# Kernel optimization log

Measured on AMD Instinct MI355X. Metric: run time of the kernel, lower is better.

## Reference

```python
import jax, jax.numpy as jnp
import numpy as np

N_NODES = 50000
N_EDGES = 800000
IN_F, H_F, OUT_F = 256, 256, 128


def setup_inputs() -> dict:
    key = jax.random.key(0)
    k1, k2, k3, k4, k5, k6 = jax.random.split(key, 6)
    in_feat = jax.random.normal(k1, (N_NODES, IN_F), dtype=jnp.float32)
    src = jax.random.randint(k2, (N_EDGES,), 0, N_NODES, dtype=jnp.int32)
    dst = jax.random.randint(k3, (N_EDGES,), 0, N_NODES, dtype=jnp.int32)
    s1 = 1.0 / np.sqrt(IN_F)
    s2 = 1.0 / np.sqrt(H_F)
    W1 = jax.random.uniform(k4, (IN_F, H_F), dtype=jnp.float32, minval=-s1, maxval=s1)
    b1 = jnp.zeros((H_F,), dtype=jnp.float32)
    W2 = jax.random.uniform(k5, (H_F, OUT_F), dtype=jnp.float32, minval=-s2, maxval=s2)
    b2 = jnp.zeros((OUT_F,), dtype=jnp.float32)
    return {"in_feat": in_feat, "src": src, "dst": dst,
            "W1": W1, "b1": b1, "W2": W2, "b2": b2}


def _graph_conv(x, W, b, src, dst, n_nodes):
    # DGL GraphConv with norm='both':
    #   h = D_in^{-1/2} A D_out^{-1/2} (X W) + b   (degrees clamped to min 1)
    ones = jnp.ones((src.shape[0],), dtype=x.dtype)
    deg_out = jax.ops.segment_sum(ones, src, num_segments=n_nodes)
    deg_in = jax.ops.segment_sum(ones, dst, num_segments=n_nodes)
    norm_out = jax.lax.rsqrt(jnp.maximum(deg_out, 1.0))  # [N]
    norm_in = jax.lax.rsqrt(jnp.maximum(deg_in, 1.0))    # [N]
    h = (x @ W) * norm_out[:, None]                       # [N, F_out]
    agg = jax.ops.segment_sum(h[src], dst, num_segments=n_nodes)  # SpMM
    return agg * norm_in[:, None] + b


def reference(in_feat, src, dst, W1, b1, W2, b2):
    n = in_feat.shape[0]
    h = _graph_conv(in_feat, W1, b1, src, dst, n)
    h = jax.nn.relu(h)
    h = _graph_conv(h, W2, b2, src, dst, n)
    # dgl.mean_nodes over a single graph -> mean across all nodes
    return jnp.mean(h, axis=0)  # [OUT_F]
```

## Files before the change

kernel.cpp:

```cpp
#include <hip/hip_runtime.h>


#define NNODES 50000
#define NEDGES 800000
#define G1_BM   ((NNODES + 127) / 128)
#define MEGA_NB 3911
#define WS_NB   4096

typedef __bf16 bf16x8 __attribute__((ext_vector_type(8)));
typedef float f32x4 __attribute__((ext_vector_type(4)));
typedef float f32x2 __attribute__((ext_vector_type(2)));

__device__ __forceinline__ unsigned short f2b(float f) {
    union { float f; unsigned u; } v; v.f = f;
    unsigned r = 0x7fffu + ((v.u >> 16) & 1u);
    return (unsigned short)((v.u + r) >> 16);
}
__device__ __forceinline__ unsigned char f2fp8(float x) {
    return (unsigned char)(__builtin_amdgcn_cvt_pk_fp8_f32(x, x, 0, false) & 0xff);
}
__device__ __forceinline__ float rdeg(int d) {
    return __frsqrt_rn((float)max(d, 1));
}

__global__ void k_cast_w1(const float* __restrict__ W1, unsigned short* __restrict__ W1t,
                          int* __restrict__ deg0) {
    int id = blockIdx.x * blockDim.x + threadIdx.x;
    int k = id >> 8, n = id & 255;
    W1t[n * 256 + k] = f2b(W1[id]);
    deg0[id] = 0;
    int j = id + 65536;
    if (j < 2 * NNODES) deg0[j] = 0;
}

__global__ __launch_bounds__(256) void k_mega1(
    const int* __restrict__ src, const int* __restrict__ dst,
    int* __restrict__ degOut, int* __restrict__ degIn,
    unsigned short* __restrict__ col2, unsigned short* __restrict__ dst2,
    const float* __restrict__ X, const unsigned short* __restrict__ W1t,
    unsigned char* __restrict__ H, int M) {
    __shared__ __align__(16) unsigned short As[128][40];
    __shared__ __align__(16) unsigned short Bs[128][40];

    int bid = blockIdx.x;
    int tid = threadIdx.x;

    if ((bid % 5) != 4) {
        int did = bid - (bid + 1) / 5;
        int e = did * 256 + tid;
        if (e < NEDGES) {
            int s = src[e], d = dst[e];
            int si = atomicAdd(&degIn[d], 1);
            if (si < 64) col2[d * 64 + si] = (unsigned short)s;
            int so = atomicAdd(&degOut[s], 1);
            if (so < 64) dst2[s * 64 + so] = (unsigned short)d;
        }
        return;
    }

    int g = bid / 5;
    int bm = g % G1_BM, bn = g / G1_BM;
    int m0 = bm * 128, n0 = bn * 128;
    int lane = tid & 63, wave = tid >> 6;
    int wm = (wave >> 1) * 64, wn = (wave & 1) * 64;
    int q = lane >> 4, r16 = lane & 15;

    f32x4 acc[4][4];
#pragma unroll
    for (int i = 0; i < 4; i++)
#pragma unroll
        for (int j = 0; j < 4; j++) acc[i][j] = 0.f;

    int c0 = tid, c1 = tid + 256;
    int r0 = c0 >> 2, k0c = (c0 & 3) * 8;
    int r1 = c1 >> 2, k1c = (c1 & 3) * 8;
    const float* Ar0 = X + (size_t)min(m0 + r0, M - 1) * 256;
    const float* Ar1 = X + (size_t)min(m0 + r1, M - 1) * 256;
    const unsigned short* Br0 = W1t + (size_t)(n0 + r0) * 256;
    const unsigned short* Br1 = W1t + (size_t)(n0 + r1) * 256;

    auto pk2u = [](float a, float b) -> unsigned {
        unsigned short x = f2b(a), y = f2b(b);
        return (unsigned)x | ((unsigned)y << 16);
    };

    for (int k0 = 0; k0 < 256; k0 += 32) {
        float4 fa0 = *(const float4*)(Ar0 + k0 + k0c);
        float4 fa1 = *(const float4*)(Ar0 + k0 + k0c + 4);
        float4 fb0 = *(const float4*)(Ar1 + k0 + k1c);
        float4 fb1 = *(const float4*)(Ar1 + k0 + k1c + 4);
        uint4 vb0 = *(const uint4*)(Br0 + k0 + k0c);
        uint4 vb1 = *(const uint4*)(Br1 + k0 + k1c);
        uint4 va0 = make_uint4(pk2u(fa0.x, fa0.y), pk2u(fa0.z, fa0.w), pk2u(fa1.x, fa1.y), pk2u(fa1.z, fa1.w));
        uint4 va1 = make_uint4(pk2u(fb0.x, fb0.y), pk2u(fb0.z, fb0.w), pk2u(fb1.x, fb1.y), pk2u(fb1.z, fb1.w));
        __syncthreads();
        *(uint4*)&As[r0][k0c] = va0;
        *(uint4*)&As[r1][k1c] = va1;
        *(uint4*)&Bs[r0][k0c] = vb0;
        *(uint4*)&Bs[r1][k1c] = vb1;
        __syncthreads();
        bf16x8 af[4], bf[4];
#pragma unroll
        for (int i = 0; i < 4; i++)
            af[i] = *(const bf16x8*)&As[wm + i * 16 + r16][q * 8];
#pragma unroll
        for (int j = 0; j < 4; j++)
            bf[j] = *(const bf16x8*)&Bs[wn + j * 16 + r16][q * 8];
#pragma unroll
        for (int i = 0; i < 4; i++)
#pragma unroll
            for (int j = 0; j < 4; j++)
                acc[i][j] = __builtin_amdgcn_mfma_f32_16x16x32_bf16(af[i], bf[j], acc[i][j], 0, 0, 0);
    }

#pragma unroll
    for (int i = 0; i < 4; i++) {
#pragma unroll
        for (int rr = 0; rr < 4; rr++) {
            int m = m0 + wm + i * 16 + q * 4 + rr;
            if (m < M) {
                unsigned char* Hp = H + (size_t)m * 256 + n0 + wn + r16;
#pragma unroll
                for (int j = 0; j < 4; j++)
                    Hp[j * 16] = f2fp8(acc[i][j][rr]);
            }
        }
    }
}

__global__ __launch_bounds__(256) void k_spmm_wsum(
    const unsigned char* __restrict__ H, const int* __restrict__ degIn,
    const int* __restrict__ degOut, const unsigned short* __restrict__ col2,
    const unsigned short* __restrict__ dst2, const float* __restrict__ bias,
    float* __restrict__ vpart) {
    __shared__ float sm[4][256];
    int wave = threadIdx.x >> 6;
    int lane = threadIdx.x & 63;
    int f = lane * 4;
    const unsigned char* Hf = H + f;
    float4 bv = *(const float4*)(bias + f);
    float vac0 = 0.f, vac1 = 0.f, vac2 = 0.f, vac3 = 0.f;

    for (int qd = blockIdx.x; qd < NNODES / 4; qd += gridDim.x) {
        int node = qd * 4 + wave;

        int dO = min(degOut[node], 64);
        float sIn = 0.f;
        if (lane < dO) sIn = rdeg(degIn[(int)dst2[node * 64 + lane]]);
#pragma unroll
        for (int o = 32; o > 0; o >>= 1) sIn += __shfl_xor(sIn, o);
        float wn = rdeg(dO) * sIn;

        int s = node * 64;
        int e = s + min(degIn[node], 64);
        float a0 = 0.f, a1 = 0.f, a2 = 0.f, a3 = 0.f;
        int i = s;
        for (; i + 16 <= e; i += 16) {
            int c[16];
#pragma unroll
            for (int u = 0; u < 16; u++) c[u] = __builtin_amdgcn_readfirstlane((int)col2[i + u]);
            float w[16]; unsigned v[16];
#pragma unroll
            for (int u = 0; u < 16; u++) {
                w[u] = rdeg(degOut[c[u]]);
                v[u] = *(const unsigned*)(Hf + (size_t)c[u] * 256);
            }
#pragma unroll
            for (int u = 0; u < 16; u++) {
                f32x2 lo = __builtin_amdgcn_cvt_pk_f32_fp8(v[u], false);
                f32x2 hi = __builtin_amdgcn_cvt_pk_f32_fp8(v[u], true);
                a0 += lo.x * w[u]; a1 += lo.y * w[u];
                a2 += hi.x * w[u]; a3 += hi.y * w[u];
            }
        }
        for (; i + 4 <= e; i += 4) {
            int c[4];
#pragma unroll
            for (int u = 0; u < 4; u++) c[u] = __builtin_amdgcn_readfirstlane((int)col2[i + u]);
            float w[4]; unsigned v[4];
#pragma unroll
            for (int u = 0; u < 4; u++) {
                w[u] = rdeg(degOut[c[u]]);
                v[u] = *(const unsigned*)(Hf + (size_t)c[u] * 256);
            }
#pragma unroll
            for (int u = 0; u < 4; u++) {
                f32x2 lo = __builtin_amdgcn_cvt_pk_f32_fp8(v[u], false);
                f32x2 hi = __builtin_amdgcn_cvt_pk_f32_fp8(v[u], true);
                a0 += lo.x * w[u]; a1 += lo.y * w[u];
                a2 += hi.x * w[u]; a3 += hi.y * w[u];
            }
        }
        for (; i < e; i++) {
            int c = __builtin_amdgcn_readfirstlane((int)col2[i]);
            float w = rdeg(degOut[c]);
            unsigned v = *(const unsigned*)(Hf + (size_t)c * 256);
            f32x2 lo = __builtin_amdgcn_cvt_pk_f32_fp8(v, false);
            f32x2 hi = __builtin_amdgcn_cvt_pk_f32_fp8(v, true);
            a0 += lo.x * w; a1 += lo.y * w;
            a2 += hi.x * w; a3 += hi.y * w;
        }
        float nm = rdeg(e - s);
        vac0 += wn * fmaxf(a0 * nm + bv.x, 0.f);
        vac1 += wn * fmaxf(a1 * nm + bv.y, 0.f);
        vac2 += wn * fmaxf(a2 * nm + bv.z, 0.f);
        vac3 += wn * fmaxf(a3 * nm + bv.w, 0.f);
    }

    *(float4*)&sm[wave][f] = make_float4(vac0, vac1, vac2, vac3);
    __syncthreads();
    int t = threadIdx.x;
    float s4 = sm[0][t] + sm[1][t] + sm[2][t] + sm[3][t];
    vpart[(size_t)blockIdx.x * 256 + t] = s4;
}

__global__ __launch_bounds__(256) void k_red1(const float* __restrict__ vpart,
                                              float* __restrict__ vred) {
    int b = blockIdx.x;
    int t = threadIdx.x;
    float s = 0.f;
    for (int i = b; i < WS_NB; i += 64) s += vpart[(size_t)i * 256 + t];
    vred[(size_t)b * 256 + t] = s;
}

__global__ __launch_bounds__(1024) void k_final(
    const float* __restrict__ vred, const float* __restrict__ W2,
    const float* __restrict__ b2, float* __restrict__ out) {
    __shared__ float part[4][256];
    __shared__ float v[256];
    int t = threadIdx.x;
    int feat = t & 255, pr = t >> 8;
    float s = 0.f;
    for (int i = pr; i < 64; i += 4) s += vred[(size_t)i * 256 + feat];
    part[pr][feat] = s;
    __syncthreads();
    if (t < 256) v[t] = part[0][t] + part[1][t] + part[2][t] + part[3][t];
    __syncthreads();
    if (t < 128) {
        float o = 0.f;
        for (int k = 0; k < 256; k++) o += v[k] * W2[k * 128 + t];
        out[t] = o * (1.0f / (float)NNODES) + b2[t];
    }
}

extern "C" void kernel_launch(void* const* d_in, const int* in_sizes, int n_in,
                              void* d_out, int out_size, void* d_ws, size_t ws_size,
                              hipStream_t stream) {
    const float* X   = (const float*)d_in[0];
    const int*   src = (const int*)d_in[1];
    const int*   dst = (const int*)d_in[2];
    const float* W1  = (const float*)d_in[3];
    const float* b1  = (const float*)d_in[4];
    const float* W2  = (const float*)d_in[5];
    const float* b2  = (const float*)d_in[6];
    float* out = (float*)d_out;

    const int n = NNODES;

    char* p = (char*)d_ws;
    auto carve = [&](size_t bytes) -> void* {
        void* r = (void*)p;
        p += (bytes + 255) & ~(size_t)255;
        return r;
    };
    int*   degOut  = (int*)carve((size_t)2 * n * sizeof(int));
    int*   degIn   = degOut + n;
    unsigned short* col2 = (unsigned short*)carve((size_t)n * 64 * 2);
    unsigned short* dst2 = (unsigned short*)carve((size_t)n * 64 * 2);
    unsigned short* W1t  = (unsigned short*)carve((size_t)256 * 256 * 2);
    unsigned char*  bufA = (unsigned char*)carve((size_t)n * 256);
    float* vpart  = (float*)carve((size_t)WS_NB * 256 * sizeof(float));
    float* vred   = (float*)carve((size_t)64 * 256 * sizeof(float));

    k_cast_w1<<<256, 256, 0, stream>>>(W1, W1t, degOut);

    k_mega1<<<MEGA_NB, 256, 0, stream>>>(src, dst, degOut, degIn, col2, dst2, X, W1t, bufA, n);

    k_spmm_wsum<<<WS_NB, 256, 0, stream>>>(bufA, degIn, degOut, col2, dst2, b1, vpart);

    k_red1<<<64, 256, 0, stream>>>(vpart, vred);
    k_final<<<1, 1024, 0, stream>>>(vred, W2, b2, out);
}
```

Baseline: 244.8 us.

## Prefetch next node's metadata and load neighbor list once per wave

The SpMM-weighted-sum kernel now loads the next iteration's degrees, column list and dst list into registers before processing the current node. Each wave reads its node's 64 column indices with one coalesced per-lane load and pulls them out with readlane, instead of issuing a scalar load per edge. The partial-sum grid is also halved, which changes the block count and the reduction size. The aim is to hide index-load latency and cut scalar memory traffic, at the cost of extra registers and fewer blocks in flight.

```diff
diff --git a/kernel.cpp b/kernel.cpp
--- a/kernel.cpp
+++ b/kernel.cpp
@@ -5,7 +5,8 @@
 #define NEDGES 800000
 #define G1_BM   ((NNODES + 127) / 128)
 #define MEGA_NB 3911
-#define WS_NB   4096
+#define WS_NB   2048
+#define NQUAD   (NNODES / 4)
 
 typedef __bf16 bf16x8 __attribute__((ext_vector_type(8)));
 typedef float f32x4 __attribute__((ext_vector_type(4)));
@@ -141,29 +142,42 @@
     float4 bv = *(const float4*)(bias + f);
     float vac0 = 0.f, vac1 = 0.f, vac2 = 0.f, vac3 = 0.f;
 
-    for (int qd = blockIdx.x; qd < NNODES / 4; qd += gridDim.x) {
-        int node = qd * 4 + wave;
-
-        int dO = min(degOut[node], 64);
+    int qd = blockIdx.x;
+    int node = qd * 4 + wave;
+    int pDI = 0, pDO = 0, pc = 0, pd = 0;
+    if (qd < NQUAD) {
+        pDI = degIn[node]; pDO = degOut[node];
+        pc = (int)col2[(size_t)node * 64 + lane];
+        pd = (int)dst2[(size_t)node * 64 + lane];
+    }
+
+    while (qd < NQUAD) {
+        int dI = min(pDI, 64), dO = min(pDO, 64);
+        int myc = pc, myd = pd;
+
+        int nqd = qd + gridDim.x;
+        if (nqd < NQUAD) {
+            int nn = nqd * 4 + wave;
+            pDI = degIn[nn]; pDO = degOut[nn];
+            pc = (int)col2[(size_t)nn * 64 + lane];
+            pd = (int)dst2[(size_t)nn * 64 + lane];
+        }
+
         float sIn = 0.f;
-        if (lane < dO) sIn = rdeg(degIn[(int)dst2[node * 64 + lane]]);
+        if (lane < dO) sIn = rdeg(degIn[myd]);
 #pragma unroll
         for (int o = 32; o > 0; o >>= 1) sIn += __shfl_xor(sIn, o);
         float wn = rdeg(dO) * sIn;
 
-        int s = node * 64;
-        int e = s + min(degIn[node], 64);
         float a0 = 0.f, a1 = 0.f, a2 = 0.f, a3 = 0.f;
-        int i = s;
-        for (; i + 16 <= e; i += 16) {
-            int c[16];
-#pragma unroll
-            for (int u = 0; u < 16; u++) c[u] = __builtin_amdgcn_readfirstlane((int)col2[i + u]);
+        int i = 0;
+        for (; i + 16 <= dI; i += 16) {
             float w[16]; unsigned v[16];
 #pragma unroll
             for (int u = 0; u < 16; u++) {
-                w[u] = rdeg(degOut[c[u]]);
-                v[u] = *(const unsigned*)(Hf + (size_t)c[u] * 256);
+                int c = __builtin_amdgcn_readlane(myc, i + u);
+                w[u] = rdeg(degOut[c]);
+                v[u] = *(const unsigned*)(Hf + (size_t)c * 256);
             }
 #pragma unroll
             for (int u = 0; u < 16; u++) {
@@ -173,15 +187,13 @@
                 a2 += hi.x * w[u]; a3 += hi.y * w[u];
             }
         }
-        for (; i + 4 <= e; i += 4) {
-            int c[4];
-#pragma unroll
-            for (int u = 0; u < 4; u++) c[u] = __builtin_amdgcn_readfirstlane((int)col2[i + u]);
+        for (; i + 4 <= dI; i += 4) {
             float w[4]; unsigned v[4];
 #pragma unroll
             for (int u = 0; u < 4; u++) {
-                w[u] = rdeg(degOut[c[u]]);
-                v[u] = *(const unsigned*)(Hf + (size_t)c[u] * 256);
+                int c = __builtin_amdgcn_readlane(myc, i + u);
+                w[u] = rdeg(degOut[c]);
+                v[u] = *(const unsigned*)(Hf + (size_t)c * 256);
             }
 #pragma unroll
             for (int u = 0; u < 4; u++) {
@@ -191,8 +203,8 @@
                 a2 += hi.x * w[u]; a3 += hi.y * w[u];
             }
         }
-        for (; i < e; i++) {
-            int c = __builtin_amdgcn_readfirstlane((int)col2[i]);
+        for (; i < dI; i++) {
+            int c = __builtin_amdgcn_readlane(myc, i);
             float w = rdeg(degOut[c]);
             unsigned v = *(const unsigned*)(Hf + (size_t)c * 256);
             f32x2 lo = __builtin_amdgcn_cvt_pk_f32_fp8(v, false);
@@ -200,11 +212,14 @@
             a0 += lo.x * w; a1 += lo.y * w;
             a2 += hi.x * w; a3 += hi.y * w;
         }
-        float nm = rdeg(e - s);
+
+        float nm = rdeg(dI);
         vac0 += wn * fmaxf(a0 * nm + bv.x, 0.f);
         vac1 += wn * fmaxf(a1 * nm + bv.y, 0.f);
         vac2 += wn * fmaxf(a2 * nm + bv.z, 0.f);
         vac3 += wn * fmaxf(a3 * nm + bv.w, 0.f);
+
+        qd = nqd;
     }
 
     *(float4*)&sm[wave][f] = make_float4(vac0, vac1, vac2, vac3);
```

After: 223.3 us. 1.1x faster.
